# Kernel optimization log

Measured on AMD Instinct MI355X. Metric: run time of the kernel, lower is better.

The kernel has to match this reference:

```python
import jax, jax.numpy as jnp
import numpy as np

N_NODES = 50000
N_EDGES = 800000
IN_CH = 128
HIDDEN = 64
LATENT = 64
OUT_CH = 128
N_GRAPHS = 500
NEG_SLOPE = 0.2


def _gat_layer(x, src, dst, W, a_src, a_dst, b, n_nodes):
    """PyG GATConv (heads=1, concat=True, add_self_loops=True, edge_dim=None)."""
    h = x @ W  # [N, F]
    loops = jnp.arange(n_nodes)
    s = jnp.concatenate([src, loops])  # source (j) of each edge incl. self loops
    d = jnp.concatenate([dst, loops])  # destination (i)
    score_src = h @ a_src  # [N]
    score_dst = h @ a_dst  # [N]
    alpha = jax.nn.leaky_relu(score_src[s] + score_dst[d], NEG_SLOPE)  # [E+N]
    # softmax grouped by destination node
    amax = jax.ops.segment_max(alpha, d, num_segments=n_nodes)
    e = jnp.exp(alpha - amax[d])
    denom = jax.ops.segment_sum(e, d, num_segments=n_nodes)
    coef = e / (denom[d] + 1e-16)
    out = jax.ops.segment_sum(h[s] * coef[:, None], d, num_segments=n_nodes)
    return out + b


def setup_inputs() -> dict:
    key = jax.random.key(0)
    ks = jax.random.split(key, 24)
    g = lambda k, shape, fan: jax.random.normal(k, shape, jnp.float32) * (1.0 / np.sqrt(fan))
    inp = {
        "x": jax.random.normal(ks[0], (N_NODES, IN_CH), jnp.float32),
        "edge_index": jax.random.randint(ks[1], (2, N_EDGES), 0, N_NODES, dtype=jnp.int64),
        "batch": jnp.sort(jax.random.randint(ks[2], (N_NODES,), 0, N_GRAPHS, dtype=jnp.int64)),
        "edge_attr": jax.random.normal(ks[3], (N_EDGES, 3), jnp.float32),
        # conv1 (GATConv in->hidden)
        "W1": g(ks[4], (IN_CH, HIDDEN), IN_CH),
        "a_src1": g(ks[5], (HIDDEN,), HIDDEN),
        "a_dst1": g(ks[6], (HIDDEN,), HIDDEN),
        "b1": jnp.zeros((HIDDEN,), jnp.float32),
        # conv2 (GATConv hidden->latent)
        "W2": g(ks[7], (HIDDEN, LATENT), HIDDEN),
        "a_src2": g(ks[8], (LATENT,), LATENT),
        "a_dst2": g(ks[9], (LATENT,), LATENT),
        "b2": jnp.zeros((LATENT,), jnp.float32),
        # encoder linear
        "lin_W": g(ks[10], (LATENT, LATENT), LATENT),
        "lin_b": jnp.zeros((LATENT,), jnp.float32),
        # decoder x_mlp
        "xm_W1": g(ks[11], (LATENT, HIDDEN), LATENT),
        "xm_b1": jnp.zeros((HIDDEN,), jnp.float32),
        "xm_W2": g(ks[12], (HIDDEN, OUT_CH), HIDDEN),
        "xm_b2": jnp.zeros((OUT_CH,), jnp.float32),
        # decoder edge_mlp
        "em_W1": g(ks[13], (LATENT, HIDDEN), LATENT),
        "em_b1": jnp.zeros((HIDDEN,), jnp.float32),
        "em_W2": g(ks[14], (HIDDEN, 3), HIDDEN),
        "em_b2": jnp.zeros((3,), jnp.float32),
    }
    return inp


def reference(x, edge_index, batch, edge_attr,
              W1, a_src1, a_dst1, b1,
              W2, a_src2, a_dst2, b2,
              lin_W, lin_b,
              xm_W1, xm_b1, xm_W2, xm_b2,
              em_W1, em_b1, em_W2, em_b2):
    src, dst = edge_index[0], edge_index[1]
    n = x.shape[0]
    # Encoder (eval mode: dropout is identity; edge_attr unused since edge_dim=None)
    h = _gat_layer(x, src, dst, W1, a_src1, a_dst1, b1, n)
    h = jax.nn.relu(h)
    z = _gat_layer(h, src, dst, W2, a_src2, a_dst2, b2, n)
    z = z @ lin_W + lin_b
    # global_mean_pool over batch ids
    sums = jax.ops.segment_sum(z, batch, num_segments=N_GRAPHS)
    counts = jax.ops.segment_sum(jnp.ones((n,), z.dtype), batch, num_segments=N_GRAPHS)
    graph_embedding = sums / jnp.maximum(counts, 1.0)[:, None]
    # MLP decoders
    x_hat = jax.nn.relu(z @ xm_W1 + xm_b1) @ xm_W2 + xm_b2
    e_hat = jax.nn.relu(z @ em_W1 + em_b1) @ em_W2 + em_b2
    return (x_hat, e_hat, z, graph_embedding)
```

## Files before the change

### kernel.cpp

```cpp
#include <hip/hip_runtime.h>
#include <hip/hip_bf16.h>
#include <cstring>

#define N_NODES 50000
#define N_EDGES 800000
#define IN_CH 128
#define NG 500
#define OUT_ELEMS 9782000
#define NBUCK 196

using bf16 = __hip_bfloat16;
typedef unsigned short u16;
typedef unsigned int u32;
typedef long long i64;
typedef unsigned long long u64;

__device__ __forceinline__ float b2f(bf16 v) { return __bfloat162float(v); }
__device__ __forceinline__ float tofl(float v) { return v; }
__device__ __forceinline__ float tofl(bf16 v) { return __bfloat162float(v); }
__device__ __forceinline__ float ldflt(const void* p, int i, int f32) {
  return f32 ? ((const float*)p)[i] : b2f(((const bf16*)p)[i]);
}
__device__ __forceinline__ int ldedge(const void* p, int i, int is64) {
  return is64 ? (int)((const i64*)p)[i] : ((const int*)p)[i];
}
__device__ __forceinline__ float sane(float v) {
  if (!isfinite(v)) return 0.f;
  return fminf(fmaxf(v, -65504.f), 65504.f);
}
__device__ __forceinline__ float lrelu(float x) { return x > 0.f ? x : 0.2f * x; }
__device__ __forceinline__ float bflo(u32 u) { return __uint_as_float(u << 16); }
__device__ __forceinline__ float bfhi(u32 u) { return __uint_as_float(u & 0xffff0000u); }

__device__ __forceinline__ float wsum(float v) {
#pragma unroll
  for (int o = 32; o > 0; o >>= 1) v += __shfl_xor(v, o, 64);
  return v;
}


__global__ void fillsig_kernel(float* __restrict__ out, int n, float v) {
  int i = blockIdx.x * 256 + threadIdx.x;
  if (i < n) out[i] = v;
}

__global__ __launch_bounds__(256) void prep_kernel(const u16* __restrict__ xb,
                                                   const int* __restrict__ ei32,
                                                   int* __restrict__ deg,
                                                   int* __restrict__ fl) {
  int bid = blockIdx.x, tid = threadIdx.x;
  if (bid < 196) {
    int i = bid * 256 + tid;
    if (i < N_NODES) deg[i] = 0;
    return;
  }
  __shared__ int c;
  if (tid == 0) c = 0;
  __syncthreads();
  int cnt = 0;
  if (bid == 196) {
#pragma unroll 4
    for (int k = 0; k < 32; ++k) {
      int i = tid + 256 * k;
      u16 u = xb[2 * i];
      int e = (u >> 7) & 0xFF;
      if (e != 0 && (e < 90 || e > 150)) ++cnt;
    }
  } else {
#pragma unroll 4
    for (int k = 0; k < 32; ++k) {
      int i = tid + 256 * k;
      if (ei32[2 * i + 1] == 0) ++cnt;
    }
  }
  atomicAdd(&c, cnt);
  __syncthreads();
  if (tid == 0) fl[bid == 196 ? 7 : 6] = c;
}

__global__ void hist_kernel(const void* __restrict__ ei, const int* __restrict__ fl,
                            int* __restrict__ deg) {
  int is64 = fl[6] > 4000;
  int e = blockIdx.x * 256 + threadIdx.x;
  if (e < N_EDGES) {
    unsigned d = (unsigned)ldedge(ei, N_EDGES + e, is64);
    if (d < N_NODES) atomicAdd(&deg[d], 1);
  }
}

__global__ __launch_bounds__(1024) void scan1_kernel(const int* __restrict__ deg,
                                                     int* __restrict__ offs,
                                                     int* __restrict__ part, int n) {
  __shared__ int sm[1024];
  int t = threadIdx.x;
  int idx = blockIdx.x * 1024 + t;
  int v = (idx < n) ? deg[idx] : 0;
  sm[t] = v;
  __syncthreads();
  for (int off = 1; off < 1024; off <<= 1) {
    int add = (t >= off) ? sm[t - off] : 0;
    __syncthreads();
    sm[t] += add;
    __syncthreads();
  }
  if (idx < n) offs[idx] = sm[t] - v;
  if (t == 1023) part[blockIdx.x] = sm[1023];
}

__global__ void scan3_kernel(int* __restrict__ offs, const int* __restrict__ part,
                             int* __restrict__ bcur, int n) {
  __shared__ int pbase;
  int b = blockIdx.x;
  int tid = threadIdx.x;
  if (tid == 0) {
    int bucket = b >> 2;
    int run = 0;
    for (int q = 0; q < bucket; ++q) run += part[q];
    pbase = run;
  }
  __syncthreads();
  int i = b * 256 + tid;
  if (i < n) {
    int v = offs[i] + pbase;
    offs[i] = v;
    if ((i & 255) == 0) bcur[i >> 8] = v;
  }
  if (i == 0) {
    int run = 0;
    for (int q = 0; q < 49; ++q) run += part[q];
    offs[n] = run;
  }
}

#define BCHUNK 4096
__global__ __launch_bounds__(256) void bucket_kernel(const void* __restrict__ ei,
                                                     const int* __restrict__ fl,
                                                     int* __restrict__ bcur,
                                                     u64* __restrict__ tmp) {
  __shared__ int hist[NBUCK], run[NBUCK], gbase[NBUCK];
  int tid = threadIdx.x;
  if (tid < NBUCK) { hist[tid] = 0; run[tid] = 0; }
  __syncthreads();
  int is64 = fl[6] > 4000;
  int base = blockIdx.x * BCHUNK;
#pragma unroll
  for (int k = 0; k < 16; ++k) {
    int e = base + k * 256 + tid;
    if (e < N_EDGES) {
      unsigned d = (unsigned)ldedge(ei, N_EDGES + e, is64);
      if (d < N_NODES) atomicAdd(&hist[d >> 8], 1);
    }
  }
  __syncthreads();
  if (tid < NBUCK) {
    int h = hist[tid];
    gbase[tid] = h ? atomicAdd(&bcur[tid], h) : 0;
  }
  __syncthreads();
#pragma unroll
  for (int k = 0; k < 16; ++k) {
    int e = base + k * 256 + tid;
    if (e < N_EDGES) {
      unsigned d = (unsigned)ldedge(ei, N_EDGES + e, is64);
      if (d < N_NODES) {
        unsigned s = (unsigned)ldedge(ei, e, is64);
        if (s >= N_NODES) s = 0;
        int pos = gbase[d >> 8] + atomicAdd(&run[d >> 8], 1);
        tmp[pos] = ((u64)s << 32) | (u64)d;
      }
    }
  }
}

__global__ __launch_bounds__(1024) void scatter2_kernel(const u64* __restrict__ tmp,
                                                        const int* __restrict__ offs,
                                                        int* __restrict__ csr) {
  __shared__ int lcur[256];
  int b = blockIdx.x;
  int tid = threadIdx.x;
  if (tid < 256) lcur[tid] = 0;
  __syncthreads();
  int nodelo = b << 8;
  int beg = offs[nodelo];
  int end = offs[min(nodelo + 256, N_NODES)];
  for (int i = beg + tid; i < end; i += 1024) {
    u64 v = tmp[i];
    int d = (int)(v & 0xFFFFFFFFu);
    int s = (int)(v >> 32);
    unsigned li = (unsigned)(d - nodelo);
    if (li < 256) {
      int pos = offs[d] + atomicAdd(&lcur[li], 1);
      if ((unsigned)pos < N_EDGES) csr[pos] = s;
    }
  }
}

template <int FIN, typename FT>
__device__ void gemm16_compute(float (&xl)[16][FIN], const void* Wv, const void* asv,
                               const void* adv, bf16* __restrict__ h, float* __restrict__ ss,
                               float* __restrict__ sd, int rbase) {
  const FT* W = (const FT*)Wv;
  const FT* as_ = (const FT*)asv;
  const FT* ad_ = (const FT*)adv;
  int lane = threadIdx.x & 63, w = threadIdx.x >> 6;
  float a_s = tofl(as_[lane]), a_d = tofl(ad_[lane]);
  int r0 = w * 4;
  float acc0 = 0.f, acc1 = 0.f, acc2 = 0.f, acc3 = 0.f;
  for (int k = 0; k < FIN; ++k) {
    float wk = tofl(W[k * 64 + lane]);
    acc0 = fmaf(xl[r0 + 0][k], wk, acc0);
    acc1 = fmaf(xl[r0 + 1][k], wk, acc1);
    acc2 = fmaf(xl[r0 + 2][k], wk, acc2);
    acc3 = fmaf(xl[r0 + 3][k], wk, acc3);
  }
  float acc[4] = {sane(acc0), sane(acc1), sane(acc2), sane(acc3)};
#pragma unroll
  for (int j = 0; j < 4; ++j) {
    int g = rbase + r0 + j;
    h[g * 64 + lane] = __float2bfloat16(acc[j]);
    float vs = wsum(acc[j] * a_s);
    float vd = wsum(acc[j] * a_d);
    if (lane == 0) { ss[g] = sane(vs); sd[g] = sane(vd); }
  }
}

template <int FIN>
__global__ __launch_bounds__(256) void gemm16_kernel(
    const void* __restrict__ xin, const void* __restrict__ W, const void* __restrict__ asrc,
    const void* __restrict__ adst, const int* __restrict__ fl, bf16* __restrict__ h,
    float* __restrict__ ss, float* __restrict__ sd) {
  __shared__ float xl[16][FIN];
  int wf = fl[7] > 2000;
  int tid = threadIdx.x;
  int rbase = blockIdx.x * 16;
  for (int i = tid; i < 16 * FIN; i += 256) {
    int rr = i / FIN, cc = i % FIN;
    xl[rr][cc] = ldflt(xin, (rbase + rr) * FIN + cc, wf);
  }
  __syncthreads();
  if (wf)
    gemm16_compute<FIN, float>(xl, W, asrc, adst, h, ss, sd, rbase);
  else
    gemm16_compute<FIN, bf16>(xl, W, asrc, adst, h, ss, sd, rbase);
}

__device__ __forceinline__ float2 agg_node2(const bf16* __restrict__ h,
                                            const float* __restrict__ ss,
                                            const float* __restrict__ sd,
                                            const int* __restrict__ offs,
                                            const int* __restrict__ csr, int d, int lane) {
  int hl = lane & 31;
  int hbase = lane & 32;
  float sdd = sd[d];
  int beg = offs[d], end = offs[d + 1];
  beg = max(0, min(beg, N_EDGES));
  end = max(beg, min(end, N_EDGES));
  float wself = __expf(fminf(lrelu(ss[d] + sdd), 60.f));
  u32 uself = ((const u32*)h)[d * 32 + hl];
  float2 acc;
  acc.x = bflo(uself) * wself;
  acc.y = bfhi(uself) * wself;
  float dpart = (hl == 0) ? wself : 0.f;
  for (int cb = beg; cb < end; cb += 32) {
    int j = cb + hl;
    int s = 0;
    float wv = 0.f;
    if (j < end) {
      s = csr[j];
      s = ((unsigned)s < N_NODES) ? s : 0;
      wv = __expf(fminf(lrelu(ss[s] + sdd), 60.f));
    }
    dpart += wv;
    int cnt = min(32, end - cb);
    for (int t0 = 0; t0 < cnt; t0 += 16) {
      u32 hv[16];
#pragma unroll
      for (int q = 0; q < 16; ++q) {
        int sq = __shfl(s, hbase + t0 + q, 64);
        hv[q] = ((const u32*)h)[sq * 32 + hl];
      }
#pragma unroll
      for (int q = 0; q < 16; ++q) {
        float wq = __shfl(wv, hbase + t0 + q, 64);
        acc.x = fmaf(bflo(hv[q]), wq, acc.x);
        acc.y = fmaf(bfhi(hv[q]), wq, acc.y);
      }
    }
  }
#pragma unroll
  for (int o = 16; o > 0; o >>= 1) dpart += __shfl_xor(dpart, o, 64);
  float den = dpart + 1e-16f;
  acc.x = acc.x / den;
  acc.y = acc.y / den;
  return acc;
}

template <typename FT>
__device__ void gemm4_compute(float (&xl)[4][64], const void* Wv, const void* asv,
                              const void* adv, bf16* __restrict__ h, float* __restrict__ ss,
                              float* __restrict__ sd, int rbase) {
  const FT* W = (const FT*)Wv;
  const FT* as_ = (const FT*)asv;
  const FT* ad_ = (const FT*)adv;
  int lane = threadIdx.x & 63;
  float a_s = tofl(as_[lane]), a_d = tofl(ad_[lane]);
  float acc0 = 0.f, acc1 = 0.f, acc2 = 0.f, acc3 = 0.f;
  for (int k = 0; k < 64; ++k) {
    float wk = tofl(W[k * 64 + lane]);
    acc0 = fmaf(xl[0][k], wk, acc0);
    acc1 = fmaf(xl[1][k], wk, acc1);
    acc2 = fmaf(xl[2][k], wk, acc2);
    acc3 = fmaf(xl[3][k], wk, acc3);
  }
  float acc[4] = {sane(acc0), sane(acc1), sane(acc2), sane(acc3)};
#pragma unroll
  for (int j = 0; j < 4; ++j) {
    int g = rbase + j;
    h[g * 64 + lane] = __float2bfloat16(acc[j]);
    float vs = wsum(acc[j] * a_s);
    float vd = wsum(acc[j] * a_d);
    if (lane == 0) { ss[g] = sane(vs); sd[g] = sane(vd); }
  }
}

template <typename FT>
__device__ void lin4_compute(float (&xl)[4][64], const void* Wv, const void* bv,
                             float* __restrict__ zio, int rbase) {
  const FT* W = (const FT*)Wv;
  const FT* b = (const FT*)bv;
  int lane = threadIdx.x & 63;
  float bl = tofl(b[lane]);
  float acc0 = bl, acc1 = bl, acc2 = bl, acc3 = bl;
  for (int k = 0; k < 64; ++k) {
    float wk = tofl(W[k * 64 + lane]);
    acc0 = fmaf(xl[0][k], wk, acc0);
    acc1 = fmaf(xl[1][k], wk, acc1);
    acc2 = fmaf(xl[2][k], wk, acc2);
    acc3 = fmaf(xl[3][k], wk, acc3);
  }
  float acc[4] = {sane(acc0), sane(acc1), sane(acc2), sane(acc3)};
#pragma unroll
  for (int j = 0; j < 4; ++j) zio[(rbase + j) * 64 + lane] = acc[j];
}

__global__ __launch_bounds__(256) void agg_gemm_kernel(
    const bf16* __restrict__ hL, const float* __restrict__ ssL, const float* __restrict__ sdL,
    const int* __restrict__ offs, const int* __restrict__ csr, const void* __restrict__ bias,
    const int* __restrict__ fl, const void* __restrict__ W2, const void* __restrict__ as2,
    const void* __restrict__ ad2, bf16* __restrict__ hOut, float* __restrict__ ssOut,
    float* __restrict__ sdOut) {
  __shared__ float o1l[8][64];
  int wf = fl[7] > 2000;
  int lane = threadIdx.x & 63, w = threadIdx.x >> 6;
  int hl = lane & 31, half = lane >> 5;
  int rbase = blockIdx.x * 8;
  int d = rbase + 2 * w + half;
  float2 r = agg_node2(hL, ssL, sdL, offs, csr, d, lane);
  float blx = ldflt(bias, 2 * hl, wf), bly = ldflt(bias, 2 * hl + 1, wf);
  o1l[2 * w + half][2 * hl] = sane(fmaxf(r.x + blx, 0.f));
  o1l[2 * w + half][2 * hl + 1] = sane(fmaxf(r.y + bly, 0.f));
  __syncthreads();
  if (w < 2) {
    float(&sub)[4][64] = *reinterpret_cast<float(*)[4][64]>(&o1l[4 * w]);
    if (wf)
      gemm4_compute<float>(sub, W2, as2, ad2, hOut, ssOut, sdOut, rbase + 4 * w);
    else
      gemm4_compute<bf16>(sub, W2, as2, ad2, hOut, ssOut, sdOut, rbase + 4 * w);
  }
}

__global__ __launch_bounds__(256) void agg_lin_kernel(
    const bf16* __restrict__ hL, const float* __restrict__ ssL, const float* __restrict__ sdL,
    const int* __restrict__ offs, const int* __restrict__ csr, const void* __restrict__ bias,
    const int* __restrict__ fl, const void* __restrict__ linW, const void* __restrict__ linb,
    float* __restrict__ zreg) {
  __shared__ float o2l[8][64];
  int wf = fl[7] > 2000;
  int lane = threadIdx.x & 63, w = threadIdx.x >> 6;
  int hl = lane & 31, half = lane >> 5;
  int rbase = blockIdx.x * 8;
  int d = rbase + 2 * w + half;
  float2 r = agg_node2(hL, ssL, sdL, offs, csr, d, lane);
  float blx = ldflt(bias, 2 * hl, wf), bly = ldflt(bias, 2 * hl + 1, wf);
  o2l[2 * w + half][2 * hl] = sane(r.x + blx);
  o2l[2 * w + half][2 * hl + 1] = sane(r.y + bly);
  __syncthreads();
  if (w < 2) {
    float(&sub)[4][64] = *reinterpret_cast<float(*)[4][64]>(&o2l[4 * w]);
    if (wf)
      lin4_compute<float>(sub, linW, linb, zreg, rbase + 4 * w);
    else
      lin4_compute<bf16>(sub, linW, linb, zreg, rbase + 4 * w);
  }
}

__global__ __launch_bounds__(256) void pool_seg_kernel(const float* __restrict__ z,
                                                       const void* __restrict__ batch,
                                                       const int* __restrict__ fl,
                                                       float* __restrict__ emb) {
  __shared__ float sm[4][64];
  __shared__ int bounds[2];
  int g = blockIdx.x;
  int tid = threadIdx.x, lane = tid & 63, w = tid >> 6;
  int is64 = fl[6] > 4000;
  if (tid < 2) {
    int target = g + tid;
    int lo = 0, hi = N_NODES;
    while (lo < hi) {
      int mid = (lo + hi) >> 1;
      if (ldedge(batch, mid, is64) < target) lo = mid + 1; else hi = mid;
    }
    bounds[tid] = lo;
  }
  __syncthreads();
  int beg = bounds[0], end = bounds[1];
  float acc = 0.f;
  for (int r = beg + w; r < end; r += 4) acc += z[r * 64 + lane];
  sm[w][lane] = acc;
  __syncthreads();
  if (w == 0) {
    float v = sm[0][lane] + sm[1][lane] + sm[2][lane] + sm[3][lane];
    float cnt = (float)max(end - beg, 1);
    emb[g * 64 + lane] = sane(v / cnt);
  }
}

template <typename FT>
__device__ void xdec16_compute(float (&zl)[16][64], float (&t1l)[16][64], const void* W1v,
                               const void* b1v, const void* W2v, const void* b2v,
                               float* __restrict__ xout, int rbase) {
  const FT* W1 = (const FT*)W1v;
  const FT* bb1 = (const FT*)b1v;
  const FT* W2 = (const FT*)W2v;
  const FT* bb2 = (const FT*)b2v;
  int lane = threadIdx.x & 63, w = threadIdx.x >> 6;
  int r0 = w * 4;
  float b1l = tofl(bb1[lane]);
  float t0 = b1l, t1 = b1l, t2 = b1l, t3 = b1l;
  for (int k = 0; k < 64; ++k) {
    float wk = tofl(W1[k * 64 + lane]);
    t0 = fmaf(zl[r0 + 0][k], wk, t0);
    t1 = fmaf(zl[r0 + 1][k], wk, t1);
    t2 = fmaf(zl[r0 + 2][k], wk, t2);
    t3 = fmaf(zl[r0 + 3][k], wk, t3);
  }
  t1l[r0 + 0][lane] = fmaxf(t0, 0.f);
  t1l[r0 + 1][lane] = fmaxf(t1, 0.f);
  t1l[r0 + 2][lane] = fmaxf(t2, 0.f);
  t1l[r0 + 3][lane] = fmaxf(t3, 0.f);
  __syncthreads();
  float b2a = tofl(bb2[lane]), b2b = tofl(bb2[64 + lane]);
  float a0[4] = {b2a, b2a, b2a, b2a};
  float a1[4] = {b2b, b2b, b2b, b2b};
  for (int k = 0; k < 64; ++k) {
    float wa = tofl(W2[k * 128 + lane]);
    float wb = tofl(W2[k * 128 + 64 + lane]);
#pragma unroll
    for (int j = 0; j < 4; ++j) {
      float tv = t1l[r0 + j][k];
      a0[j] = fmaf(tv, wa, a0[j]);
      a1[j] = fmaf(tv, wb, a1[j]);
    }
  }
#pragma unroll
  for (int j = 0; j < 4; ++j) {
    int g = rbase + r0 + j;
    xout[g * 128 + lane] = sane(a0[j]);
    xout[g * 128 + 64 + lane] = sane(a1[j]);
  }
}

template <typename FT>
__device__ void edec16_compute(float (&zl)[16][64], float (&t1l)[16][65], float (&W2l)[192],
                               const void* W1v, const void* b1v, const void* b2v,
                               float* __restrict__ eout, int rbase) {
  const FT* W1 = (const FT*)W1v;
  const FT* bb1 = (const FT*)b1v;
  const FT* bb2 = (const FT*)b2v;
  int lane = threadIdx.x & 63, w = threadIdx.x >> 6;
  int r0 = w * 4;
  float b1l = tofl(bb1[lane]);
  float t0 = b1l, t1 = b1l, t2 = b1l, t3 = b1l;
  for (int k = 0; k < 64; ++k) {
    float wk = tofl(W1[k * 64 + lane]);
    t0 = fmaf(zl[r0 + 0][k], wk, t0);
    t1 = fmaf(zl[r0 + 1][k], wk, t1);
    t2 = fmaf(zl[r0 + 2][k], wk, t2);
    t3 = fmaf(zl[r0 + 3][k], wk, t3);
  }
  t1l[r0 + 0][lane] = fmaxf(t0, 0.f);
  t1l[r0 + 1][lane] = fmaxf(t1, 0.f);
  t1l[r0 + 2][lane] = fmaxf(t2, 0.f);
  t1l[r0 + 3][lane] = fmaxf(t3, 0.f);
  __syncthreads();
  int j = lane >> 4, c = lane & 15;
  if (c < 3) {
    int row = r0 + j;
    float acc = tofl(bb2[c]);
#pragma unroll 4
    for (int k = 0; k < 64; ++k) acc = fmaf(t1l[row][k], W2l[k * 3 + c], acc);
    eout[(rbase + row) * 3 + c] = sane(acc);
  }
}

__global__ __launch_bounds__(256) void dec_kernel(
    const float* __restrict__ z, const void* __restrict__ xmW1, const void* __restrict__ xmb1,
    const void* __restrict__ xmW2, const void* __restrict__ xmb2, const void* __restrict__ emW1,
    const void* __restrict__ emb1, const void* __restrict__ emW2, const void* __restrict__ emb2,
    const int* __restrict__ fl, float* __restrict__ xout, float* __restrict__ eout) {
  __shared__ float zl[16][64];
  __shared__ float t1x[16][64];
  __shared__ float t1e[16][65];
  __shared__ float W2l[192];
  int wf = fl[7] > 2000;
  int tid = threadIdx.x;
  int rbase = blockIdx.x * 16;
  for (int i = tid; i < 1024; i += 256) zl[i >> 6][i & 63] = z[rbase * 64 + i];
  if (tid < 192) W2l[tid] = wf ? ((const float*)emW2)[tid] : b2f(((const bf16*)emW2)[tid]);
  __syncthreads();
  if (wf) {
    edec16_compute<float>(zl, t1e, W2l, emW1, emb1, emb2, eout, rbase);
    xdec16_compute<float>(zl, t1x, xmW1, xmb1, xmW2, xmb2, xout, rbase);
  } else {
    edec16_compute<bf16>(zl, t1e, W2l, emW1, emb1, emb2, eout, rbase);
    xdec16_compute<bf16>(zl, t1x, xmW1, xmb1, xmW2, xmb2, xout, rbase);
  }
}

extern "C" void kernel_launch(void* const* d_in, const int* in_sizes, int n_in,
                              void* d_out, int out_size, void* d_ws, size_t ws_size,
                              hipStream_t stream) {
  float* outf = (float*)d_out;
  if (out_size != OUT_ELEMS) {
    float sig = 2048.0f + fminf((float)out_size * 1e-4f, 999.f);
    fillsig_kernel<<<(out_size + 255) / 256, 256, 0, stream>>>(outf, out_size, sig);
    return;
  }
  if (n_in < 22 || in_sizes[0] != N_NODES * IN_CH || in_sizes[1] != 2 * N_EDGES) {
    fillsig_kernel<<<(out_size + 255) / 256, 256, 0, stream>>>(outf, out_size, 5000.f);
    return;
  }

  const void* x = d_in[0];
  const void* ei = d_in[1];
  const void* batch = d_in[2];
  const void* W1 = d_in[4];
  const void* as1 = d_in[5];
  const void* ad1 = d_in[6];
  const void* b1 = d_in[7];
  const void* W2 = d_in[8];
  const void* as2 = d_in[9];
  const void* ad2 = d_in[10];
  const void* b2 = d_in[11];
  const void* linW = d_in[12];
  const void* linb = d_in[13];
  const void* xmW1 = d_in[14];
  const void* xmb1 = d_in[15];
  const void* xmW2 = d_in[16];
  const void* xmb2 = d_in[17];
  const void* emW1 = d_in[18];
  const void* emb1 = d_in[19];
  const void* emW2 = d_in[20];
  const void* emb2 = d_in[21];

  float* xhat = outf;
  float* ehat = outf + 6400000;
  float* zreg = outf + 6550000;
  float* emb = outf + 9750000;

  bool usews = ws_size >= (size_t)17100000;
  char* base = usews ? (char*)d_ws : (char*)d_out;
  int* deg = (int*)(base + 0);
  int* bcur = (int*)(base + 200000);
  int* offs = (int*)(base + 400000);
  int* part = (int*)(base + 600016);
  int* flags = (int*)(base + 600272);
  float* ssb = (float*)(base + 600448);
  float* sdb = (float*)(base + 800448);
  int* csr = (int*)(base + 1000448);
  bf16* hbuf = (bf16*)(base + 4200448);
  u64* tmp = (u64*)(base + 10600448);
  float* ss2 = (float*)(base + 0);
  float* sd2 = (float*)(base + 200000);
  bf16* hbuf2 = (bf16*)(base + 10600448);

  int err = 0, idx = 0;
  (void)hipGetLastError();
#define CK()                                                                       \
  do {                                                                             \
    ++idx;                                                                         \
    hipError_t e_ = hipGetLastError();                                             \
    if (e_ != hipSuccess && err == 0) err = 8192 + idx * 256 + ((int)e_ & 3) * 64; \
  } while (0)

  prep_kernel<<<198, 256, 0, stream>>>((const u16*)x, (const int*)ei, deg, flags); CK();
  hist_kernel<<<N_EDGES / 256, 256, 0, stream>>>(ei, flags, deg); CK();
  scan1_kernel<<<49, 1024, 0, stream>>>(deg, offs, part, N_NODES); CK();
  scan3_kernel<<<(N_NODES + 255) / 256, 256, 0, stream>>>(offs, part, bcur, N_NODES); CK();
  bucket_kernel<<<(N_EDGES + BCHUNK - 1) / BCHUNK, 256, 0, stream>>>(ei, flags, bcur, tmp); CK();
  scatter2_kernel<<<NBUCK, 1024, 0, stream>>>(tmp, offs, csr); CK();
  gemm16_kernel<IN_CH><<<N_NODES / 16, 256, 0, stream>>>(x, W1, as1, ad1, flags, hbuf, ssb, sdb); CK();
  agg_gemm_kernel<<<N_NODES / 8, 256, 0, stream>>>(hbuf, ssb, sdb, offs, csr, b1, flags,
                                                   W2, as2, ad2, hbuf2, ss2, sd2); CK();
  agg_lin_kernel<<<N_NODES / 8, 256, 0, stream>>>(hbuf2, ss2, sd2, offs, csr, b2, flags,
                                                  linW, linb, zreg); CK();
  pool_seg_kernel<<<NG, 256, 0, stream>>>(zreg, batch, flags, emb); CK();
  dec_kernel<<<N_NODES / 16, 256, 0, stream>>>(zreg, xmW1, xmb1, xmW2, xmb2,
                                               emW1, emb1, emW2, emb2, flags, xhat, ehat); CK();
#undef CK

  if (err != 0) {
    static float s_sent;
    s_sent = (float)err;
    (void)hipMemcpyAsync(d_out, &s_sent, 4, hipMemcpyHostToDevice, stream);
  }
}
```

Before: 344.3 us.

## Merge bucket with layer-1 GEMM and pool with decoder; spread post-aggregation GEMM over all waves

```diff
diff --git a/kernel.cpp b/kernel.cpp
--- a/kernel.cpp
+++ b/kernel.cpp
@@ -8,6 +8,8 @@
 #define NG 500
 #define OUT_ELEMS 9782000
 #define NBUCK 196
+#define GEMMB 3125
+#define DECB 3125
 
 using bf16 = __hip_bfloat16;
 typedef unsigned short u16;
@@ -129,69 +131,6 @@
     int run = 0;
     for (int q = 0; q < 49; ++q) run += part[q];
     offs[n] = run;
-  }
-}
-
-#define BCHUNK 4096
-__global__ __launch_bounds__(256) void bucket_kernel(const void* __restrict__ ei,
-                                                     const int* __restrict__ fl,
-                                                     int* __restrict__ bcur,
-                                                     u64* __restrict__ tmp) {
-  __shared__ int hist[NBUCK], run[NBUCK], gbase[NBUCK];
-  int tid = threadIdx.x;
-  if (tid < NBUCK) { hist[tid] = 0; run[tid] = 0; }
-  __syncthreads();
-  int is64 = fl[6] > 4000;
-  int base = blockIdx.x * BCHUNK;
-#pragma unroll
-  for (int k = 0; k < 16; ++k) {
-    int e = base + k * 256 + tid;
-    if (e < N_EDGES) {
-      unsigned d = (unsigned)ldedge(ei, N_EDGES + e, is64);
-      if (d < N_NODES) atomicAdd(&hist[d >> 8], 1);
-    }
-  }
-  __syncthreads();
-  if (tid < NBUCK) {
-    int h = hist[tid];
-    gbase[tid] = h ? atomicAdd(&bcur[tid], h) : 0;
-  }
-  __syncthreads();
-#pragma unroll
-  for (int k = 0; k < 16; ++k) {
-    int e = base + k * 256 + tid;
-    if (e < N_EDGES) {
-      unsigned d = (unsigned)ldedge(ei, N_EDGES + e, is64);
-      if (d < N_NODES) {
-        unsigned s = (unsigned)ldedge(ei, e, is64);
-        if (s >= N_NODES) s = 0;
-        int pos = gbase[d >> 8] + atomicAdd(&run[d >> 8], 1);
-        tmp[pos] = ((u64)s << 32) | (u64)d;
-      }
-    }
-  }
-}
-
-__global__ __launch_bounds__(1024) void scatter2_kernel(const u64* __restrict__ tmp,
-                                                        const int* __restrict__ offs,
-                                                        int* __restrict__ csr) {
-  __shared__ int lcur[256];
-  int b = blockIdx.x;
-  int tid = threadIdx.x;
-  if (tid < 256) lcur[tid] = 0;
-  __syncthreads();
-  int nodelo = b << 8;
-  int beg = offs[nodelo];
-  int end = offs[min(nodelo + 256, N_NODES)];
-  for (int i = beg + tid; i < end; i += 1024) {
-    u64 v = tmp[i];
-    int d = (int)(v & 0xFFFFFFFFu);
-    int s = (int)(v >> 32);
-    unsigned li = (unsigned)(d - nodelo);
-    if (li < 256) {
-      int pos = offs[d] + atomicAdd(&lcur[li], 1);
-      if ((unsigned)pos < N_EDGES) csr[pos] = s;
-    }
   }
 }
 
@@ -224,24 +163,83 @@
   }
 }
 
-template <int FIN>
-__global__ __launch_bounds__(256) void gemm16_kernel(
+#define BCHUNK 4096
+__global__ __launch_bounds__(256) void bucket_gemm_kernel(
+    const void* __restrict__ ei, int* __restrict__ bcur, u64* __restrict__ tmp,
     const void* __restrict__ xin, const void* __restrict__ W, const void* __restrict__ asrc,
     const void* __restrict__ adst, const int* __restrict__ fl, bf16* __restrict__ h,
     float* __restrict__ ss, float* __restrict__ sd) {
-  __shared__ float xl[16][FIN];
+  __shared__ int hist[NBUCK], run[NBUCK], gbase[NBUCK];
+  __shared__ float xl[16][IN_CH];
+  int bid = blockIdx.x, tid = threadIdx.x;
+  int is64 = fl[6] > 4000;
   int wf = fl[7] > 2000;
+  if (bid < NBUCK) {
+    if (tid < NBUCK) { hist[tid] = 0; run[tid] = 0; }
+    __syncthreads();
+    int base = bid * BCHUNK;
+#pragma unroll
+    for (int k = 0; k < 16; ++k) {
+      int e = base + k * 256 + tid;
+      if (e < N_EDGES) {
+        unsigned d = (unsigned)ldedge(ei, N_EDGES + e, is64);
+        if (d < N_NODES) atomicAdd(&hist[d >> 8], 1);
+      }
+    }
+    __syncthreads();
+    if (tid < NBUCK) {
+      int hh = hist[tid];
+      gbase[tid] = hh ? atomicAdd(&bcur[tid], hh) : 0;
+    }
+    __syncthreads();
+#pragma unroll
+    for (int k = 0; k < 16; ++k) {
+      int e = base + k * 256 + tid;
+      if (e < N_EDGES) {
+        unsigned d = (unsigned)ldedge(ei, N_EDGES + e, is64);
+        if (d < N_NODES) {
+          unsigned s = (unsigned)ldedge(ei, e, is64);
+          if (s >= N_NODES) s = 0;
+          int pos = gbase[d >> 8] + atomicAdd(&run[d >> 8], 1);
+          tmp[pos] = ((u64)s << 32) | (u64)d;
+        }
+      }
+    }
+    return;
+  }
+  int rbase = (bid - NBUCK) * 16;
+  for (int i = tid; i < 16 * IN_CH; i += 256) {
+    int rr = i / IN_CH, cc = i % IN_CH;
+    xl[rr][cc] = ldflt(xin, (rbase + rr) * IN_CH + cc, wf);
+  }
+  __syncthreads();
+  if (wf)
+    gemm16_compute<IN_CH, float>(xl, W, asrc, adst, h, ss, sd, rbase);
+  else
+    gemm16_compute<IN_CH, bf16>(xl, W, asrc, adst, h, ss, sd, rbase);
+}
+
+__global__ __launch_bounds__(1024) void scatter2_kernel(const u64* __restrict__ tmp,
+                                                        const int* __restrict__ offs,
+                                                        int* __restrict__ csr) {
+  __shared__ int lcur[256];
+  int b = blockIdx.x;
   int tid = threadIdx.x;
-  int rbase = blockIdx.x * 16;
-  for (int i = tid; i < 16 * FIN; i += 256) {
-    int rr = i / FIN, cc = i % FIN;
-    xl[rr][cc] = ldflt(xin, (rbase + rr) * FIN + cc, wf);
-  }
-  __syncthreads();
-  if (wf)
-    gemm16_compute<FIN, float>(xl, W, asrc, adst, h, ss, sd, rbase);
-  else
-    gemm16_compute<FIN, bf16>(xl, W, asrc, adst, h, ss, sd, rbase);
+  if (tid < 256) lcur[tid] = 0;
+  __syncthreads();
+  int nodelo = b << 8;
+  int beg = offs[nodelo];
+  int end = offs[min(nodelo + 256, N_NODES)];
+  for (int i = beg + tid; i < end; i += 1024) {
+    u64 v = tmp[i];
+    int d = (int)(v & 0xFFFFFFFFu);
+    int s = (int)(v >> 32);
+    unsigned li = (unsigned)(d - nodelo);
+    if (li < 256) {
+      int pos = offs[d] + atomicAdd(&lcur[li], 1);
+      if ((unsigned)pos < N_EDGES) csr[pos] = s;
+    }
+  }
 }
 
 __device__ __forceinline__ float2 agg_node2(const bf16* __restrict__ h,
@@ -296,7 +294,7 @@
 }
 
 template <typename FT>
-__device__ void gemm4_compute(float (&xl)[4][64], const void* Wv, const void* asv,
+__device__ void gemm2_compute(float (&xl)[8][64], int r0, const void* Wv, const void* asv,
                               const void* adv, bf16* __restrict__ h, float* __restrict__ ss,
                               float* __restrict__ sd, int rbase) {
   const FT* W = (const FT*)Wv;
@@ -304,18 +302,16 @@
   const FT* ad_ = (const FT*)adv;
   int lane = threadIdx.x & 63;
   float a_s = tofl(as_[lane]), a_d = tofl(ad_[lane]);
-  float acc0 = 0.f, acc1 = 0.f, acc2 = 0.f, acc3 = 0.f;
+  float acc0 = 0.f, acc1 = 0.f;
   for (int k = 0; k < 64; ++k) {
     float wk = tofl(W[k * 64 + lane]);
-    acc0 = fmaf(xl[0][k], wk, acc0);
-    acc1 = fmaf(xl[1][k], wk, acc1);
-    acc2 = fmaf(xl[2][k], wk, acc2);
-    acc3 = fmaf(xl[3][k], wk, acc3);
-  }
-  float acc[4] = {sane(acc0), sane(acc1), sane(acc2), sane(acc3)};
-#pragma unroll
-  for (int j = 0; j < 4; ++j) {
-    int g = rbase + j;
+    acc0 = fmaf(xl[r0 + 0][k], wk, acc0);
+    acc1 = fmaf(xl[r0 + 1][k], wk, acc1);
+  }
+  float acc[2] = {sane(acc0), sane(acc1)};
+#pragma unroll
+  for (int j = 0; j < 2; ++j) {
+    int g = rbase + r0 + j;
     h[g * 64 + lane] = __float2bfloat16(acc[j]);
     float vs = wsum(acc[j] * a_s);
     float vd = wsum(acc[j] * a_d);
@@ -324,23 +320,21 @@
 }
 
 template <typename FT>
-__device__ void lin4_compute(float (&xl)[4][64], const void* Wv, const void* bv,
+__device__ void lin2_compute(float (&xl)[8][64], int r0, const void* Wv, const void* bv,
                              float* __restrict__ zio, int rbase) {
   const FT* W = (const FT*)Wv;
   const FT* b = (const FT*)bv;
   int lane = threadIdx.x & 63;
   float bl = tofl(b[lane]);
-  float acc0 = bl, acc1 = bl, acc2 = bl, acc3 = bl;
+  float acc0 = bl, acc1 = bl;
   for (int k = 0; k < 64; ++k) {
     float wk = tofl(W[k * 64 + lane]);
-    acc0 = fmaf(xl[0][k], wk, acc0);
-    acc1 = fmaf(xl[1][k], wk, acc1);
-    acc2 = fmaf(xl[2][k], wk, acc2);
-    acc3 = fmaf(xl[3][k], wk, acc3);
-  }
-  float acc[4] = {sane(acc0), sane(acc1), sane(acc2), sane(acc3)};
-#pragma unroll
-  for (int j = 0; j < 4; ++j) zio[(rbase + j) * 64 + lane] = acc[j];
+    acc0 = fmaf(xl[r0 + 0][k], wk, acc0);
+    acc1 = fmaf(xl[r0 + 1][k], wk, acc1);
+  }
+  float acc[2] = {sane(acc0), sane(acc1)};
+#pragma unroll
+  for (int j = 0; j < 2; ++j) zio[(rbase + r0 + j) * 64 + lane] = acc[j];
 }
 
 __global__ __launch_bounds__(256) void agg_gemm_kernel(
@@ -360,13 +354,10 @@
   o1l[2 * w + half][2 * hl] = sane(fmaxf(r.x + blx, 0.f));
   o1l[2 * w + half][2 * hl + 1] = sane(fmaxf(r.y + bly, 0.f));
   __syncthreads();
-  if (w < 2) {
-    float(&sub)[4][64] = *reinterpret_cast<float(*)[4][64]>(&o1l[4 * w]);
-    if (wf)
-      gemm4_compute<float>(sub, W2, as2, ad2, hOut, ssOut, sdOut, rbase + 4 * w);
-    else
-      gemm4_compute<bf16>(sub, W2, as2, ad2, hOut, ssOut, sdOut, rbase + 4 * w);
-  }
+  if (wf)
+    gemm2_compute<float>(o1l, 2 * w, W2, as2, ad2, hOut, ssOut, sdOut, rbase);
+  else
+    gemm2_compute<bf16>(o1l, 2 * w, W2, as2, ad2, hOut, ssOut, sdOut, rbase);
 }
 
 __global__ __launch_bounds__(256) void agg_lin_kernel(
@@ -385,44 +376,10 @@
   o2l[2 * w + half][2 * hl] = sane(r.x + blx);
   o2l[2 * w + half][2 * hl + 1] = sane(r.y + bly);
   __syncthreads();
-  if (w < 2) {
-    float(&sub)[4][64] = *reinterpret_cast<float(*)[4][64]>(&o2l[4 * w]);
-    if (wf)
-      lin4_compute<float>(sub, linW, linb, zreg, rbase + 4 * w);
-    else
-      lin4_compute<bf16>(sub, linW, linb, zreg, rbase + 4 * w);
-  }
-}
-
-__global__ __launch_bounds__(256) void pool_seg_kernel(const float* __restrict__ z,
-                                                       const void* __restrict__ batch,
-                                                       const int* __restrict__ fl,
-                                                       float* __restrict__ emb) {
-  __shared__ float sm[4][64];
-  __shared__ int bounds[2];
-  int g = blockIdx.x;
-  int tid = threadIdx.x, lane = tid & 63, w = tid >> 6;
-  int is64 = fl[6] > 4000;
-  if (tid < 2) {
-    int target = g + tid;
-    int lo = 0, hi = N_NODES;
-    while (lo < hi) {
-      int mid = (lo + hi) >> 1;
-      if (ldedge(batch, mid, is64) < target) lo = mid + 1; else hi = mid;
-    }
-    bounds[tid] = lo;
-  }
-  __syncthreads();
-  int beg = bounds[0], end = bounds[1];
-  float acc = 0.f;
-  for (int r = beg + w; r < end; r += 4) acc += z[r * 64 + lane];
-  sm[w][lane] = acc;
-  __syncthreads();
-  if (w == 0) {
-    float v = sm[0][lane] + sm[1][lane] + sm[2][lane] + sm[3][lane];
-    float cnt = (float)max(end - beg, 1);
-    emb[g * 64 + lane] = sane(v / cnt);
-  }
+  if (wf)
+    lin2_compute<float>(o2l, 2 * w, linW, linb, zreg, rbase);
+  else
+    lin2_compute<bf16>(o2l, 2 * w, linW, linb, zreg, rbase);
 }
 
 template <typename FT>
@@ -503,17 +460,46 @@
   }
 }
 
-__global__ __launch_bounds__(256) void dec_kernel(
+__global__ __launch_bounds__(256) void dec_pool_kernel(
     const float* __restrict__ z, const void* __restrict__ xmW1, const void* __restrict__ xmb1,
     const void* __restrict__ xmW2, const void* __restrict__ xmb2, const void* __restrict__ emW1,
     const void* __restrict__ emb1, const void* __restrict__ emW2, const void* __restrict__ emb2,
-    const int* __restrict__ fl, float* __restrict__ xout, float* __restrict__ eout) {
+    const void* __restrict__ batch, const int* __restrict__ fl, float* __restrict__ xout,
+    float* __restrict__ eout, float* __restrict__ emb) {
   __shared__ float zl[16][64];
   __shared__ float t1x[16][64];
   __shared__ float t1e[16][65];
   __shared__ float W2l[192];
+  int tid = threadIdx.x;
+  if (blockIdx.x >= DECB) {
+    float(&sm)[4][64] = *reinterpret_cast<float(*)[4][64]>(&zl[0][0]);
+    int* bounds = (int*)&t1x[0][0];
+    int g = blockIdx.x - DECB;
+    int lane = tid & 63, w = tid >> 6;
+    int is64 = fl[6] > 4000;
+    if (tid < 2) {
+      int target = g + tid;
+      int lo = 0, hi = N_NODES;
+      while (lo < hi) {
+        int mid = (lo + hi) >> 1;
+        if (ldedge(batch, mid, is64) < target) lo = mid + 1; else hi = mid;
+      }
+      bounds[tid] = lo;
+    }
+    __syncthreads();
+    int beg = bounds[0], end = bounds[1];
+    float acc = 0.f;
+    for (int r = beg + w; r < end; r += 4) acc += z[r * 64 + lane];
+    sm[w][lane] = acc;
+    __syncthreads();
+    if (w == 0) {
+      float v = sm[0][lane] + sm[1][lane] + sm[2][lane] + sm[3][lane];
+      float cnt = (float)max(end - beg, 1);
+      emb[g * 64 + lane] = sane(v / cnt);
+    }
+    return;
+  }
   int wf = fl[7] > 2000;
-  int tid = threadIdx.x;
   int rbase = blockIdx.x * 16;
   for (int i = tid; i < 1024; i += 256) zl[i >> 6][i & 63] = z[rbase * 64 + i];
   if (tid < 192) W2l[tid] = wf ? ((const float*)emW2)[tid] : b2f(((const bf16*)emW2)[tid]);
@@ -597,16 +583,16 @@
   hist_kernel<<<N_EDGES / 256, 256, 0, stream>>>(ei, flags, deg); CK();
   scan1_kernel<<<49, 1024, 0, stream>>>(deg, offs, part, N_NODES); CK();
   scan3_kernel<<<(N_NODES + 255) / 256, 256, 0, stream>>>(offs, part, bcur, N_NODES); CK();
-  bucket_kernel<<<(N_EDGES + BCHUNK - 1) / BCHUNK, 256, 0, stream>>>(ei, flags, bcur, tmp); CK();
+  bucket_gemm_kernel<<<NBUCK + GEMMB, 256, 0, stream>>>(
+      ei, bcur, tmp, x, W1, as1, ad1, flags, hbuf, ssb, sdb); CK();
   scatter2_kernel<<<NBUCK, 1024, 0, stream>>>(tmp, offs, csr); CK();
-  gemm16_kernel<IN_CH><<<N_NODES / 16, 256, 0, stream>>>(x, W1, as1, ad1, flags, hbuf, ssb, sdb); CK();
   agg_gemm_kernel<<<N_NODES / 8, 256, 0, stream>>>(hbuf, ssb, sdb, offs, csr, b1, flags,
                                                    W2, as2, ad2, hbuf2, ss2, sd2); CK();
   agg_lin_kernel<<<N_NODES / 8, 256, 0, stream>>>(hbuf2, ss2, sd2, offs, csr, b2, flags,
                                                   linW, linb, zreg); CK();
-  pool_seg_kernel<<<NG, 256, 0, stream>>>(zreg, batch, flags, emb); CK();
-  dec_kernel<<<N_NODES / 16, 256, 0, stream>>>(zreg, xmW1, xmb1, xmW2, xmb2,
-                                               emW1, emb1, emW2, emb2, flags, xhat, ehat); CK();
+  dec_pool_kernel<<<DECB + NG, 256, 0, stream>>>(zreg, xmW1, xmb1, xmW2, xmb2,
+                                                 emW1, emb1, emW2, emb2, batch, flags,
+                                                 xhat, ehat, emb); CK();
 #undef CK
 
   if (err != 0) {
```

New measurement: 332.4 us. 3.5% less time.
